# Performance work log

Measured on AMD Instinct MI355X. Metric: run time of the kernel, lower is better.

## Reference

```python
import jax, jax.numpy as jnp
import numpy as np

N_NODES = 100000
FEATURES, HIDDEN, CLASSES = 256, 128, 32
N_EDGES = 1600000


def setup_inputs() -> dict:
    key = jax.random.key(0)
    k1, k2, k3, k4, k5 = jax.random.split(key, 5)
    x = jax.random.normal(k1, (N_NODES, FEATURES), dtype=jnp.float32)
    edge_index = jax.random.randint(k2, (2, N_EDGES), 0, N_NODES, dtype=jnp.int64)
    # GCNConv: Linear(in, out, bias=False) + separate bias added after aggregation
    s1 = 1.0 / np.sqrt(FEATURES)
    s2 = 1.0 / np.sqrt(HIDDEN)
    W1 = jax.random.uniform(k3, (FEATURES, HIDDEN), jnp.float32, -s1, s1)
    b1 = jnp.zeros((HIDDEN,), jnp.float32)
    W2 = jax.random.uniform(k4, (HIDDEN, CLASSES), jnp.float32, -s2, s2)
    b2 = jnp.zeros((CLASSES,), jnp.float32)
    return {"x": x, "W1": W1, "b1": b1, "W2": W2, "b2": b2, "edge_index": edge_index}


def _gcn_conv(x, edge_index, W, b, n_nodes):
    # PyG GCNConv with add_self_loops=False: out = D^{-1/2} A D^{-1/2} (X W) + b
    src, dst = edge_index[0], edge_index[1]
    h = x @ W  # [N, out]
    deg = jax.ops.segment_sum(jnp.ones_like(dst, dtype=h.dtype), dst, num_segments=n_nodes)
    dinv = jnp.where(deg > 0, jax.lax.rsqrt(jnp.maximum(deg, 1e-12)), 0.0)
    norm = dinv[src] * dinv[dst]  # [E]
    msgs = h[src] * norm[:, None]  # [E, out] gather + scale
    out = jax.ops.segment_sum(msgs, dst, num_segments=n_nodes)  # scatter-add
    return out + b


def reference(x, W1, b1, W2, b2, edge_index):
    h = _gcn_conv(x, edge_index, W1, b1, N_NODES)
    h = jax.nn.relu(h)
    # F.dropout(training=self.training): eval mode -> identity
    h = _gcn_conv(h, edge_index, W2, b2, N_NODES)
    return jax.nn.log_softmax(h, axis=1)
```

## Files before the change

### kernel.cpp

```cpp
#include <hip/hip_runtime.h>

typedef unsigned short u16;
typedef unsigned int   u32;
typedef __attribute__((ext_vector_type(8))) short short8;
typedef __attribute__((ext_vector_type(4))) float f32x4;

constexpr int BSH = 9;
constexpr int BSZ = 1 << BSH;

__device__ inline float bf2f(u32 bits16) {
    union { u32 u; float f; } c; c.u = bits16 << 16; return c.f;
}
__device__ inline u16 f2bf(float f) {
    union { float f; u32 u; } c; c.f = f;
    return (u16)((c.u + 0x8000u) >> 16);
}
__device__ inline int ld_edge(const void* eb, int f64, size_t idx) {
    return f64 ? (int)((const long long*)eb)[idx] : ((const int*)eb)[idx];
}

__global__ void detect_kernel(const u32* xw, const int* ebuf_int, int* flags) {
    __shared__ int cnt;
    if (threadIdx.x == 0) cnt = 0;
    __syncthreads();
    u32 w = xw[threadIdx.x];
    int e = (int)((w >> 7) & 0xffu);
    if (e >= 110 && e <= 145) atomicAdd(&cnt, 1);
    int ev = ebuf_int[2 * threadIdx.x + 1];
    unsigned long long any = __ballot(ev != 0);
    __syncthreads();
    if (threadIdx.x == 0) {
        flags[0] = (cnt < 192) ? 1 : 0;
        flags[1] = 0;
        flags[2] = (any == 0ULL) ? 1 : 0;
    }
}

__global__ void bconv_kernel(const void* b1, const void* b2, const int* flags,
                             float* b1f, float* b2f, int HID, int CLS) {
    int i = blockIdx.x * 256 + threadIdx.x;
    int f = flags[0];
    if (i < HID) b1f[i] = f ? ((const float*)b1)[i] : bf2f(((const u16*)b1)[i]);
    if (i < CLS) b2f[i] = f ? ((const float*)b2)[i] : bf2f(((const u16*)b2)[i]);
}

__global__ void hist_kernel(const void* eb, const int* flags, int* bucket_cnt,
                            int E, int nb) {
    __shared__ int hist[256];
    hist[threadIdx.x] = 0;
    __syncthreads();
    int f64 = flags[2];
    int base = blockIdx.x * 4096;
    #pragma unroll
    for (int k = 0; k < 16; ++k) {
        int e = base + k * 256 + threadIdx.x;
        if (e < E) {
            int d = ld_edge(eb, f64, (size_t)E + e);
            atomicAdd(&hist[d >> BSH], 1);
        }
    }
    __syncthreads();
    int b = threadIdx.x;
    if (b < nb) { int c = hist[b]; if (c) atomicAdd(&bucket_cnt[b], c); }
}

__global__ void bucket_scan_kernel(const int* bucket_cnt, int* bucket_base,
                                   int* bucket_rsv, int nb, int E) {
    __shared__ int wsum[4];
    int t = threadIdx.x, lane = t & 63, wv = t >> 6;
    int v = (t < nb) ? bucket_cnt[t] : 0;
    int inc = v;
    #pragma unroll
    for (int d = 1; d < 64; d <<= 1) {
        int tmp = __shfl_up(inc, d, 64);
        if (lane >= d) inc += tmp;
    }
    if (lane == 63) wsum[wv] = inc;
    __syncthreads();
    int off = 0;
    #pragma unroll
    for (int w = 0; w < 4; ++w) if (w < wv) off += wsum[w];
    int excl = off + inc - v;
    if (t <= nb) bucket_base[t] = (t == nb) ? E : excl;
    if (t < nb) bucket_rsv[t] = excl;
}

__global__ __launch_bounds__(256)
void passA_kernel(const void* eb, const int* flags, int* bucket_rsv,
                  int* bsrc, int* bdst, int E, int nb) {
    __shared__ int hist[256];
    __shared__ int rbase[256];
    hist[threadIdx.x] = 0;
    __syncthreads();
    int f64 = flags[2];
    int base = blockIdx.x * 8192;
    #pragma unroll
    for (int k = 0; k < 32; ++k) {
        int e = base + k * 256 + threadIdx.x;
        if (e < E) {
            int d = ld_edge(eb, f64, (size_t)E + e);
            atomicAdd(&hist[d >> BSH], 1);
        }
    }
    __syncthreads();
    {
        int b = threadIdx.x;
        int c = (b < nb) ? hist[b] : 0;
        rbase[b] = c ? atomicAdd(&bucket_rsv[b], c) : 0;
        hist[b] = 0;
    }
    __syncthreads();
    #pragma unroll
    for (int k = 0; k < 32; ++k) {
        int e = base + k * 256 + threadIdx.x;
        if (e < E) {
            int d = ld_edge(eb, f64, (size_t)E + e);
            int s = ld_edge(eb, f64, (size_t)e);
            int bb = d >> BSH;
            int r = atomicAdd(&hist[bb], 1);
            int pos = rbase[bb] + r;
            bsrc[pos] = s;
            bdst[pos] = d;
        }
    }
}

__global__ __launch_bounds__(256)
void degB_kernel(const int* bdst, const int* bucket_base, int* deg, float* dinv, int N) {
    __shared__ int cur[BSZ];
    int b = blockIdx.x, d0 = b << BSH;
    for (int i = threadIdx.x; i < BSZ; i += 256) cur[i] = 0;
    __syncthreads();
    int e0 = bucket_base[b], e1 = bucket_base[b + 1];
    for (int e = e0 + threadIdx.x; e < e1; e += 256)
        atomicAdd(&cur[bdst[e] - d0], 1);
    __syncthreads();
    for (int i = threadIdx.x; i < BSZ; i += 256) {
        int d = d0 + i;
        if (d < N) {
            int c = cur[i];
            deg[d] = c;
            dinv[d] = (c > 0) ? 1.0f / sqrtf((float)c) : 0.0f;
        }
    }
}

__global__ __launch_bounds__(256)
void passB_kernel(const int* bsrc, const int* bdst, const int* bucket_base,
                  const int* row_start, int* csr) {
    __shared__ int cur[BSZ];
    int b = blockIdx.x, d0 = b << BSH;
    for (int i = threadIdx.x; i < BSZ; i += 256) cur[i] = 0;
    __syncthreads();
    int e0 = bucket_base[b], e1 = bucket_base[b + 1];
    for (int e = e0 + threadIdx.x; e < e1; e += 256) {
        int d = bdst[e];
        int s = bsrc[e];
        int r = atomicAdd(&cur[d - d0], 1);
        csr[row_start[d] + r] = s;
    }
}

__device__ inline int wave_incl_scan(int v, int lane) {
    #pragma unroll
    for (int d = 1; d < 64; d <<= 1) {
        int t = __shfl_up(v, d, 64);
        if (lane >= d) v += t;
    }
    return v;
}

__global__ void scan_block_kernel(const int* deg, int* row_start, int* bsums, int N) {
    __shared__ int wsum[4];
    int t = threadIdx.x, lane = t & 63, wv = t >> 6;
    int i = blockIdx.x * 256 + t;
    int v = (i < N) ? deg[i] : 0;
    int inc = wave_incl_scan(v, lane);
    if (lane == 63) wsum[wv] = inc;
    __syncthreads();
    int off = 0;
    #pragma unroll
    for (int w = 0; w < 4; ++w) if (w < wv) off += wsum[w];
    if (i < N) row_start[i] = off + inc - v;
    if (t == 255) bsums[blockIdx.x] = off + inc;
}

__global__ void scan_sums_kernel(int* bsums, int nb) {
    __shared__ int wsum[8];
    int t = threadIdx.x, lane = t & 63, wv = t >> 6;
    int v = (t < nb) ? bsums[t] : 0;
    int inc = wave_incl_scan(v, lane);
    if (lane == 63) wsum[wv] = inc;
    __syncthreads();
    int off = 0;
    #pragma unroll
    for (int w = 0; w < 8; ++w) if (w < wv) off += wsum[w];
    if (t < nb) bsums[t] = off + inc - v;
}

__global__ void scan_add_kernel(int* row_start, const int* bsums, int N, int E) {
    int i = blockIdx.x * 256 + threadIdx.x;
    if (i < N) row_start[i] += bsums[blockIdx.x];
    if (blockIdx.x == 0 && threadIdx.x == 0) row_start[N] = E;
}

template<int NT, int KT, int NCOLS>
__global__ void prepack_kernel(const void* W, const int* flags, u16* pack) {
    int p = blockIdx.x * 256 + threadIdx.x;
    constexpr int TOT = NT * KT * 64 * 8;
    if (p >= TOT) return;
    int j = p & 7, lane = (p >> 3) & 63, fk = p >> 9;
    int kk = fk % KT, nt = fk / KT;
    int n = nt * 16 + (lane & 15);
    int k = kk * 32 + (lane >> 4) * 8 + j;
    u16 v = flags[0] ? f2bf(((const float*)W)[k * NCOLS + n])
                     : ((const u16*)W)[k * NCOLS + n];
    pack[p] = v;
}

template<int NT, int KT, int G>
__global__ __launch_bounds__(256)
void gemm_kernel(const void* __restrict__ A, const int* __restrict__ ff,
                 const u16* __restrict__ Bpack, const float* __restrict__ dinv,
                 u16* __restrict__ C, int M) {
    constexpr int K = KT * 32;
    constexpr int Ncols = NT * 16;
    __shared__ short8 lds[NT * KT * 64];
    for (int i = threadIdx.x; i < NT * KT * 64; i += 256)
        lds[i] = ((const short8*)Bpack)[i];
    bool fA = (*ff != 0);
    __syncthreads();
    int wave = threadIdx.x >> 6, lane = threadIdx.x & 63;
    int m0 = (blockIdx.x * 4 + wave) * (16 * G);
    if (m0 >= M) return;
    int q = lane >> 4;
    int rowc[G];
    #pragma unroll
    for (int g = 0; g < G; ++g) {
        int r = m0 + g * 16 + (lane & 15);
        rowc[g] = (r < M) ? r : (M - 1);
    }
    f32x4 acc[G][NT];
    #pragma unroll
    for (int g = 0; g < G; ++g)
        #pragma unroll
        for (int nt = 0; nt < NT; ++nt) acc[g][nt] = (f32x4){0.f, 0.f, 0.f, 0.f};
    #pragma unroll
    for (int kk = 0; kk < KT; ++kk) {
        short8 a[G];
        #pragma unroll
        for (int g = 0; g < G; ++g) {
            if (fA) {
                const float* Af = (const float*)A + (size_t)rowc[g] * K + kk * 32 + q * 8;
                f32x4 v0 = ((const f32x4*)Af)[0];
                f32x4 v1 = ((const f32x4*)Af)[1];
                union { short8 s; u16 u[8]; } pa;
                pa.u[0] = f2bf(v0[0]); pa.u[1] = f2bf(v0[1]);
                pa.u[2] = f2bf(v0[2]); pa.u[3] = f2bf(v0[3]);
                pa.u[4] = f2bf(v1[0]); pa.u[5] = f2bf(v1[1]);
                pa.u[6] = f2bf(v1[2]); pa.u[7] = f2bf(v1[3]);
                a[g] = pa.s;
            } else {
                a[g] = ((const short8*)((const u16*)A + (size_t)rowc[g] * K))[kk * 4 + q];
            }
        }
        #pragma unroll
        for (int nt = 0; nt < NT; ++nt) {
            short8 b = lds[(nt * KT + kk) * 64 + lane];
            #pragma unroll
            for (int g = 0; g < G; ++g)
                acc[g][nt] = __builtin_amdgcn_mfma_f32_16x16x32_bf16(a[g], b, acc[g][nt], 0, 0, 0);
        }
    }
    #pragma unroll
    for (int g = 0; g < G; ++g) {
        float sc[4];
        #pragma unroll
        for (int r = 0; r < 4; ++r) {
            int rr = m0 + g * 16 + q * 4 + r;
            sc[r] = dinv[(rr < M) ? rr : (M - 1)];
        }
        #pragma unroll
        for (int nt = 0; nt < NT; ++nt) {
            int col = nt * 16 + (lane & 15);
            #pragma unroll
            for (int r = 0; r < 4; ++r) {
                int rrow = m0 + g * 16 + q * 4 + r;
                if (rrow < M)
                    C[(size_t)rrow * Ncols + col] = f2bf(acc[g][nt][r] * sc[r]);
            }
        }
    }
}

__global__ __launch_bounds__(256)
void agg1_kernel(const u32* __restrict__ H32, const int* __restrict__ csr,
                 const int* __restrict__ row_start, const float* __restrict__ dinv,
                 const float* __restrict__ b1f, u32* __restrict__ H1, int N) {
    int wave = threadIdx.x >> 6, lane = threadIdx.x & 63;
    int n = blockIdx.x * 4 + wave;
    if (n >= N) return;
    int s0 = row_start[n], s1 = row_start[n + 1];
    float acc0 = 0.f, acc1 = 0.f;
    for (int base = s0; base < s1; base += 64) {
        int m = s1 - base; if (m > 64) m = 64;
        int myidx = (lane < m) ? csr[base + lane] : 0;
        int j = 0;
        for (; j + 4 <= m; j += 4) {
            int i0 = __shfl(myidx, j);
            int i1 = __shfl(myidx, j + 1);
            int i2 = __shfl(myidx, j + 2);
            int i3 = __shfl(myidx, j + 3);
            u32 h0 = H32[(size_t)i0 * 64 + lane];
            u32 h1 = H32[(size_t)i1 * 64 + lane];
            u32 h2 = H32[(size_t)i2 * 64 + lane];
            u32 h3 = H32[(size_t)i3 * 64 + lane];
            acc0 += bf2f(h0 & 0xffffu); acc1 += bf2f(h0 >> 16);
            acc0 += bf2f(h1 & 0xffffu); acc1 += bf2f(h1 >> 16);
            acc0 += bf2f(h2 & 0xffffu); acc1 += bf2f(h2 >> 16);
            acc0 += bf2f(h3 & 0xffffu); acc1 += bf2f(h3 >> 16);
        }
        for (; j < m; ++j) {
            int s = __shfl(myidx, j);
            u32 h = H32[(size_t)s * 64 + lane];
            acc0 += bf2f(h & 0xffffu); acc1 += bf2f(h >> 16);
        }
    }
    float wn = dinv[n];
    float v0 = fmaxf(wn * acc0 + b1f[2 * lane], 0.f);
    float v1 = fmaxf(wn * acc1 + b1f[2 * lane + 1], 0.f);
    H1[(size_t)n * 64 + lane] = (u32)f2bf(v0) | ((u32)f2bf(v1) << 16);
}

__global__ __launch_bounds__(256)
void agg2_kernel(const u16* __restrict__ H2, const int* __restrict__ csr,
                 const int* __restrict__ row_start, const float* __restrict__ dinv,
                 const float* __restrict__ b2f, const int* __restrict__ ff,
                 void* __restrict__ out, int N) {
    int half = threadIdx.x >> 5;
    int c = threadIdx.x & 31;
    int n = blockIdx.x * 8 + half;
    if (n >= N) return;
    int s0 = row_start[n], s1 = row_start[n + 1];
    float acc = 0.f;
    for (int base = s0; base < s1; base += 32) {
        int m = s1 - base; if (m > 32) m = 32;
        int myidx = (c < m) ? csr[base + c] : 0;
        int j = 0;
        for (; j + 4 <= m; j += 4) {
            int i0 = __shfl(myidx, j, 32);
            int i1 = __shfl(myidx, j + 1, 32);
            int i2 = __shfl(myidx, j + 2, 32);
            int i3 = __shfl(myidx, j + 3, 32);
            float h0 = bf2f(H2[(size_t)i0 * 32 + c]);
            float h1 = bf2f(H2[(size_t)i1 * 32 + c]);
            float h2 = bf2f(H2[(size_t)i2 * 32 + c]);
            float h3 = bf2f(H2[(size_t)i3 * 32 + c]);
            acc += h0 + h1 + h2 + h3;
        }
        for (; j < m; ++j) {
            int s = __shfl(myidx, j, 32);
            acc += bf2f(H2[(size_t)s * 32 + c]);
        }
    }
    float tot = dinv[n] * acc + b2f[c];
    float mx = tot;
    #pragma unroll
    for (int m = 16; m; m >>= 1) mx = fmaxf(mx, __shfl_xor(mx, m, 32));
    float ex = expf(tot - mx);
    float sm = ex;
    #pragma unroll
    for (int m = 16; m; m >>= 1) sm += __shfl_xor(sm, m, 32);
    float r = tot - mx - logf(sm);
    if (*ff) ((float*)out)[(size_t)n * 32 + c] = r;
    else     ((u16*)out)[(size_t)n * 32 + c] = f2bf(r);
}

extern "C" void kernel_launch(void* const* d_in, const int* in_sizes, int n_in,
                              void* d_out, int out_size, void* d_ws, size_t ws_size,
                              hipStream_t stream) {
    const void* x  = d_in[0];
    const void* W1 = d_in[1];
    const void* b1 = d_in[2];
    const void* W2 = d_in[3];
    const void* b2 = d_in[4];
    const void* eb = d_in[5];

    const int HID  = in_sizes[2];
    const int CLS  = in_sizes[4];
    const int FEAT = in_sizes[1] / HID;
    const int N    = in_sizes[0] / FEAT;
    const int E    = in_sizes[5] / 2;
    const int nb   = (N + BSZ - 1) >> BSH;
    (void)n_in; (void)out_size;

    char* w = (char*)d_ws;
    size_t p = 0;
    auto alloc = [&](size_t bytes) {
        size_t o = p; p = (p + bytes + 255) & ~(size_t)255; return o;
    };
    int*   flags      = (int*)  (w + alloc(32));
    int*   deg        = (int*)  (w + alloc((size_t)N * 4));
    int*   row_start  = (int*)  (w + alloc((size_t)(N + 1) * 4));
    int*   bsums      = (int*)  (w + alloc(512 * 4));
    int*   bucket_cnt = (int*)  (w + alloc(257 * 4));
    int*   bucket_base= (int*)  (w + alloc(257 * 4));
    int*   bucket_rsv = (int*)  (w + alloc(256 * 4));
    int*   bsrc       = (int*)  (w + alloc((size_t)E * 4));
    int*   bdst       = (int*)  (w + alloc((size_t)E * 4));
    int*   csr        = (int*)  (w + alloc((size_t)E * 4));
    float* dinv       = (float*)(w + alloc((size_t)N * 4));
    float* b1f        = (float*)(w + alloc((size_t)HID * 4));
    float* b2f        = (float*)(w + alloc((size_t)CLS * 4));
    u16*   B1p        = (u16*)  (w + alloc((size_t)FEAT * HID * 2));
    u16*   B2p        = (u16*)  (w + alloc((size_t)HID * CLS * 2));
    u16*   H          = (u16*)  (w + alloc((size_t)N * HID * 2));
    u16*   H1         = (u16*)  (w + alloc((size_t)N * HID * 2));
    u16*   H2         = (u16*)  (w + alloc((size_t)N * CLS * 2));
    if (p > ws_size) return;

    detect_kernel<<<1, 256, 0, stream>>>((const u32*)x, (const int*)eb, flags);
    hipMemsetAsync(bucket_cnt, 0, 257 * 4, stream);
    bconv_kernel<<<1, 256, 0, stream>>>(b1, b2, flags, b1f, b2f, HID, CLS);

    hist_kernel<<<(E + 4095) / 4096, 256, 0, stream>>>(eb, flags, bucket_cnt, E, nb);
    bucket_scan_kernel<<<1, 256, 0, stream>>>(bucket_cnt, bucket_base, bucket_rsv, nb, E);
    passA_kernel<<<(E + 8191) / 8192, 256, 0, stream>>>(eb, flags, bucket_rsv,
                                                        bsrc, bdst, E, nb);
    degB_kernel<<<nb, 256, 0, stream>>>(bdst, bucket_base, deg, dinv, N);

    int nsb = (N + 255) / 256;
    scan_block_kernel<<<nsb, 256, 0, stream>>>(deg, row_start, bsums, N);
    scan_sums_kernel<<<1, 512, 0, stream>>>(bsums, nsb);
    scan_add_kernel<<<nsb, 256, 0, stream>>>(row_start, bsums, N, E);

    passB_kernel<<<nb, 256, 0, stream>>>(bsrc, bdst, bucket_base, row_start, csr);

    prepack_kernel<8, 8, 128><<<(8 * 8 * 64 * 8 + 255) / 256, 256, 0, stream>>>(W1, flags, B1p);
    prepack_kernel<2, 4, 32><<<(2 * 4 * 64 * 8 + 255) / 256, 256, 0, stream>>>(W2, flags, B2p);

    int gblocks = (N + 127) / 128;
    gemm_kernel<8, 8, 2><<<gblocks, 256, 0, stream>>>(x, flags, B1p, dinv, H, N);
    agg1_kernel<<<(N + 3) / 4, 256, 0, stream>>>((const u32*)H, csr, row_start, dinv, b1f,
                                                 (u32*)H1, N);
    gemm_kernel<2, 4, 2><<<gblocks, 256, 0, stream>>>(H1, flags + 1, B2p, dinv, H2, N);
    agg2_kernel<<<(N + 7) / 8, 256, 0, stream>>>(H2, csr, row_start, dinv, b2f, flags,
                                                 (void*)d_out, N);
}
```

Measured before the change: 401.2 us.

## Double-buffer first-layer GEMM with async global-to-LDS loads per K-slice

Replaces the first GEMM with a new kernel that stages A and B tiles per 32-wide K slice into double-buffered LDS using global_load_lds async copies, overlapping the next slice's loads with MFMA on the current one. W1 is repacked in K-major order so each K slice of B is contiguous. The goal is to hide global memory latency of the large x read, which dominates the first GEMM. It adds more LDS use and a barrier per K step, and depends on correct async-copy layout.

```diff
diff --git a/kernel.cpp b/kernel.cpp
--- a/kernel.cpp
+++ b/kernel.cpp
@@ -17,6 +17,11 @@
 }
 __device__ inline int ld_edge(const void* eb, int f64, size_t idx) {
     return f64 ? (int)((const long long*)eb)[idx] : ((const int*)eb)[idx];
+}
+__device__ inline void async_cp16(const void* g, void* s) {
+    __builtin_amdgcn_global_load_lds(
+        (const __attribute__((address_space(1))) unsigned int*)g,
+        (__attribute__((address_space(3))) unsigned int*)s, 16, 0, 0);
 }
 
 __global__ void detect_kernel(const u32* xw, const int* ebuf_int, int* flags) {
@@ -216,6 +221,127 @@
     u16 v = flags[0] ? f2bf(((const float*)W)[k * NCOLS + n])
                      : ((const u16*)W)[k * NCOLS + n];
     pack[p] = v;
+}
+
+template<int NT, int KT, int NCOLS>
+__global__ void prepackK_kernel(const void* W, const int* flags, u16* pack) {
+    int p = blockIdx.x * 256 + threadIdx.x;
+    constexpr int TOT = NT * KT * 64 * 8;
+    if (p >= TOT) return;
+    int j = p & 7, lane = (p >> 3) & 63, fk = p >> 9;
+    int nt = fk % NT, kk = fk / NT;
+    int n = nt * 16 + (lane & 15);
+    int k = kk * 32 + (lane >> 4) * 8 + j;
+    u16 v = flags[0] ? f2bf(((const float*)W)[k * NCOLS + n])
+                     : ((const u16*)W)[k * NCOLS + n];
+    pack[p] = v;
+}
+
+template<int NT, int KT>
+__global__ __launch_bounds__(256)
+void gemm1_kernel(const void* __restrict__ A, const int* __restrict__ ff,
+                  const u16* __restrict__ Bpack, const float* __restrict__ dinv,
+                  u16* __restrict__ C, int M) {
+    constexpr int K = KT * 32;
+    constexpr int Ncols = NT * 16;
+    __shared__ char As[2][16384];
+    __shared__ char Bs[2][8192];
+    const bool fA = (*ff != 0);
+    const int wave = threadIdx.x >> 6, lane = threadIdx.x & 63;
+    const int r0 = blockIdx.x * 128;
+
+    auto stage = [&](int kk, int buf) {
+        if (fA) {
+            #pragma unroll
+            for (int i = 0; i < 4; ++i) {
+                int cb = (i * 4 + wave) * 32;
+                int c = cb + (lane >> 1);
+                int rg = c >> 6, rem = c & 63, q = rem >> 4, l16 = rem & 15;
+                int row = r0 + rg * 16 + l16; if (row >= M) row = M - 1;
+                const char* g = (const char*)A + (size_t)row * (K * 4)
+                                + (kk * 32 + q * 8) * 4 + (lane & 1) * 16;
+                async_cp16(g, &As[buf][(size_t)cb * 32]);
+            }
+        } else {
+            #pragma unroll
+            for (int i = 0; i < 2; ++i) {
+                int cb = (i * 4 + wave) * 64;
+                int c = cb + lane;
+                int rg = c >> 6, rem = c & 63, q = rem >> 4, l16 = rem & 15;
+                int row = r0 + rg * 16 + l16; if (row >= M) row = M - 1;
+                const char* g = (const char*)A + (size_t)row * (K * 2)
+                                + (kk * 32 + q * 8) * 2;
+                async_cp16(g, &As[buf][(size_t)cb * 16]);
+            }
+        }
+        #pragma unroll
+        for (int i = 0; i < 2; ++i) {
+            int off = (i * 4 + wave) * 1024;
+            const char* g = (const char*)Bpack + (size_t)kk * (NT * 1024) + off
+                            + (size_t)lane * 16;
+            async_cp16(g, &Bs[buf][off]);
+        }
+    };
+
+    const int q = lane >> 4, l16 = lane & 15;
+    f32x4 acc[2][NT];
+    #pragma unroll
+    for (int g = 0; g < 2; ++g)
+        #pragma unroll
+        for (int nt = 0; nt < NT; ++nt) acc[g][nt] = (f32x4){0.f, 0.f, 0.f, 0.f};
+
+    stage(0, 0);
+    #pragma unroll
+    for (int kk = 0; kk < KT; ++kk) {
+        int cur = kk & 1;
+        __syncthreads();
+        if (kk + 1 < KT) stage(kk + 1, cur ^ 1);
+        short8 a[2];
+        #pragma unroll
+        for (int g = 0; g < 2; ++g) {
+            int rg = wave * 2 + g;
+            int fragidx = (rg * 4 + q) * 16 + l16;
+            if (fA) {
+                const f32x4* ap = (const f32x4*)&As[cur][(size_t)fragidx * 32];
+                f32x4 v0 = ap[0];
+                f32x4 v1 = ap[1];
+                union { short8 s; u16 u[8]; } pa;
+                pa.u[0] = f2bf(v0[0]); pa.u[1] = f2bf(v0[1]);
+                pa.u[2] = f2bf(v0[2]); pa.u[3] = f2bf(v0[3]);
+                pa.u[4] = f2bf(v1[0]); pa.u[5] = f2bf(v1[1]);
+                pa.u[6] = f2bf(v1[2]); pa.u[7] = f2bf(v1[3]);
+                a[g] = pa.s;
+            } else {
+                a[g] = *(const short8*)&As[cur][(size_t)fragidx * 16];
+            }
+        }
+        #pragma unroll
+        for (int nt = 0; nt < NT; ++nt) {
+            short8 b = ((const short8*)Bs[cur])[nt * 64 + lane];
+            acc[0][nt] = __builtin_amdgcn_mfma_f32_16x16x32_bf16(a[0], b, acc[0][nt], 0, 0, 0);
+            acc[1][nt] = __builtin_amdgcn_mfma_f32_16x16x32_bf16(a[1], b, acc[1][nt], 0, 0, 0);
+        }
+    }
+    #pragma unroll
+    for (int g = 0; g < 2; ++g) {
+        int mg = r0 + (wave * 2 + g) * 16;
+        float sc[4];
+        #pragma unroll
+        for (int r = 0; r < 4; ++r) {
+            int rr = mg + q * 4 + r;
+            sc[r] = dinv[(rr < M) ? rr : (M - 1)];
+        }
+        #pragma unroll
+        for (int nt = 0; nt < NT; ++nt) {
+            int col = nt * 16 + l16;
+            #pragma unroll
+            for (int r = 0; r < 4; ++r) {
+                int rrow = mg + q * 4 + r;
+                if (rrow < M)
+                    C[(size_t)rrow * Ncols + col] = f2bf(acc[g][nt][r] * sc[r]);
+            }
+        }
+    }
 }
 
 template<int NT, int KT, int G>
@@ -436,14 +562,13 @@
 
     passB_kernel<<<nb, 256, 0, stream>>>(bsrc, bdst, bucket_base, row_start, csr);
 
-    prepack_kernel<8, 8, 128><<<(8 * 8 * 64 * 8 + 255) / 256, 256, 0, stream>>>(W1, flags, B1p);
+    prepackK_kernel<8, 8, 128><<<(8 * 8 * 64 * 8 + 255) / 256, 256, 0, stream>>>(W1, flags, B1p);
     prepack_kernel<2, 4, 32><<<(2 * 4 * 64 * 8 + 255) / 256, 256, 0, stream>>>(W2, flags, B2p);
 
-    int gblocks = (N + 127) / 128;
-    gemm_kernel<8, 8, 2><<<gblocks, 256, 0, stream>>>(x, flags, B1p, dinv, H, N);
+    gemm1_kernel<8, 8><<<(N + 127) / 128, 256, 0, stream>>>(x, flags, B1p, dinv, H, N);
     agg1_kernel<<<(N + 3) / 4, 256, 0, stream>>>((const u32*)H, csr, row_start, dinv, b1f,
                                                  (u32*)H1, N);
-    gemm_kernel<2, 4, 2><<<gblocks, 256, 0, stream>>>(H1, flags + 1, B2p, dinv, H2, N);
+    gemm_kernel<2, 4, 2><<<(N + 127) / 128, 256, 0, stream>>>(H1, flags + 1, B2p, dinv, H2, N);
     agg2_kernel<<<(N + 7) / 8, 256, 0, stream>>>(H2, csr, row_start, dinv, b2f, flags,
                                                  (void*)d_out, N);
 }
```

After: 397.9 us. No clear change (-0.8%).

## Split first GEMM across column halves and unroll aggregation gathers deeper

Applied to the files above, without the earlier changes.

The first GEMM now runs as gemm1_kernel, which splits the 128 output columns into two halves handled by separate blocks. This doubles the grid and halves the LDS footprint per block, meant to raise occupancy, but each block re-reads its A rows, so the x reads are duplicated. Both aggregation kernels gain an 8-way unrolled gather loop to keep more loads in flight. agg1 also uses a packed float2 bf16 unpack with tree-style sums, which slightly changes the floating-point summation order.

```diff
diff --git a/kernel.cpp b/kernel.cpp
--- a/kernel.cpp
+++ b/kernel.cpp
@@ -4,6 +4,7 @@
 typedef unsigned int   u32;
 typedef __attribute__((ext_vector_type(8))) short short8;
 typedef __attribute__((ext_vector_type(4))) float f32x4;
+typedef __attribute__((ext_vector_type(2))) float f32x2;
 
 constexpr int BSH = 9;
 constexpr int BSZ = 1 << BSH;
@@ -14,6 +15,12 @@
 __device__ inline u16 f2bf(float f) {
     union { float f; u32 u; } c; c.f = f;
     return (u16)((c.u + 0x8000u) >> 16);
+}
+__device__ inline f32x2 up2(u32 h) {
+    union { u32 u[2]; f32x2 f; } c;
+    c.u[0] = h << 16;
+    c.u[1] = h & 0xffff0000u;
+    return c.f;
 }
 __device__ inline int ld_edge(const void* eb, int f64, size_t idx) {
     return f64 ? (int)((const long long*)eb)[idx] : ((const int*)eb)[idx];
@@ -218,26 +225,33 @@
     pack[p] = v;
 }
 
-template<int NT, int KT, int G>
-__global__ __launch_bounds__(256)
-void gemm_kernel(const void* __restrict__ A, const int* __restrict__ ff,
-                 const u16* __restrict__ Bpack, const float* __restrict__ dinv,
-                 u16* __restrict__ C, int M) {
+template<int NT, int NTF, int KT, int G>
+__global__ __launch_bounds__(256)
+void gemm1_kernel(const void* __restrict__ A, const int* __restrict__ ff,
+                  const u16* __restrict__ Bpack, const float* __restrict__ dinv,
+                  u16* __restrict__ C, int M) {
     constexpr int K = KT * 32;
-    constexpr int Ncols = NT * 16;
+    constexpr int Ncols = NTF * 16;
+    constexpr int NSPLIT = NTF / NT;
     __shared__ short8 lds[NT * KT * 64];
-    for (int i = threadIdx.x; i < NT * KT * 64; i += 256)
-        lds[i] = ((const short8*)Bpack)[i];
+    const int bh = blockIdx.x % NSPLIT;
+    const int bm = blockIdx.x / NSPLIT;
+    for (int i = threadIdx.x; i < NT * KT * 64; i += 256) {
+        int lane_ = i & 63;
+        int kk = (i >> 6) % KT;
+        int nt = (i >> 6) / KT;
+        lds[i] = ((const short8*)Bpack)[(((bh * NT + nt) * KT) + kk) * 64 + lane_];
+    }
     bool fA = (*ff != 0);
     __syncthreads();
     int wave = threadIdx.x >> 6, lane = threadIdx.x & 63;
-    int m0 = (blockIdx.x * 4 + wave) * (16 * G);
+    int m0 = (bm * 4 + wave) * (16 * G);
     if (m0 >= M) return;
-    int q = lane >> 4;
+    int q = lane >> 4, l16 = lane & 15;
     int rowc[G];
     #pragma unroll
     for (int g = 0; g < G; ++g) {
-        int r = m0 + g * 16 + (lane & 15);
+        int r = m0 + g * 16 + l16;
         rowc[g] = (r < M) ? r : (M - 1);
     }
     f32x4 acc[G][NT];
@@ -282,6 +296,81 @@
         }
         #pragma unroll
         for (int nt = 0; nt < NT; ++nt) {
+            int col = bh * (NT * 16) + nt * 16 + l16;
+            #pragma unroll
+            for (int r = 0; r < 4; ++r) {
+                int rrow = m0 + g * 16 + q * 4 + r;
+                if (rrow < M)
+                    C[(size_t)rrow * Ncols + col] = f2bf(acc[g][nt][r] * sc[r]);
+            }
+        }
+    }
+}
+
+template<int NT, int KT, int G>
+__global__ __launch_bounds__(256)
+void gemm_kernel(const void* __restrict__ A, const int* __restrict__ ff,
+                 const u16* __restrict__ Bpack, const float* __restrict__ dinv,
+                 u16* __restrict__ C, int M) {
+    constexpr int K = KT * 32;
+    constexpr int Ncols = NT * 16;
+    __shared__ short8 lds[NT * KT * 64];
+    for (int i = threadIdx.x; i < NT * KT * 64; i += 256)
+        lds[i] = ((const short8*)Bpack)[i];
+    bool fA = (*ff != 0);
+    __syncthreads();
+    int wave = threadIdx.x >> 6, lane = threadIdx.x & 63;
+    int m0 = (blockIdx.x * 4 + wave) * (16 * G);
+    if (m0 >= M) return;
+    int q = lane >> 4;
+    int rowc[G];
+    #pragma unroll
+    for (int g = 0; g < G; ++g) {
+        int r = m0 + g * 16 + (lane & 15);
+        rowc[g] = (r < M) ? r : (M - 1);
+    }
+    f32x4 acc[G][NT];
+    #pragma unroll
+    for (int g = 0; g < G; ++g)
+        #pragma unroll
+        for (int nt = 0; nt < NT; ++nt) acc[g][nt] = (f32x4){0.f, 0.f, 0.f, 0.f};
+    #pragma unroll
+    for (int kk = 0; kk < KT; ++kk) {
+        short8 a[G];
+        #pragma unroll
+        for (int g = 0; g < G; ++g) {
+            if (fA) {
+                const float* Af = (const float*)A + (size_t)rowc[g] * K + kk * 32 + q * 8;
+                f32x4 v0 = ((const f32x4*)Af)[0];
+                f32x4 v1 = ((const f32x4*)Af)[1];
+                union { short8 s; u16 u[8]; } pa;
+                pa.u[0] = f2bf(v0[0]); pa.u[1] = f2bf(v0[1]);
+                pa.u[2] = f2bf(v0[2]); pa.u[3] = f2bf(v0[3]);
+                pa.u[4] = f2bf(v1[0]); pa.u[5] = f2bf(v1[1]);
+                pa.u[6] = f2bf(v1[2]); pa.u[7] = f2bf(v1[3]);
+                a[g] = pa.s;
+            } else {
+                a[g] = ((const short8*)((const u16*)A + (size_t)rowc[g] * K))[kk * 4 + q];
+            }
+        }
+        #pragma unroll
+        for (int nt = 0; nt < NT; ++nt) {
+            short8 b = lds[(nt * KT + kk) * 64 + lane];
+            #pragma unroll
+            for (int g = 0; g < G; ++g)
+                acc[g][nt] = __builtin_amdgcn_mfma_f32_16x16x32_bf16(a[g], b, acc[g][nt], 0, 0, 0);
+        }
+    }
+    #pragma unroll
+    for (int g = 0; g < G; ++g) {
+        float sc[4];
+        #pragma unroll
+        for (int r = 0; r < 4; ++r) {
+            int rr = m0 + g * 16 + q * 4 + r;
+            sc[r] = dinv[(rr < M) ? rr : (M - 1)];
+        }
+        #pragma unroll
+        for (int nt = 0; nt < NT; ++nt) {
             int col = nt * 16 + (lane & 15);
             #pragma unroll
             for (int r = 0; r < 4; ++r) {
@@ -301,11 +390,34 @@
     int n = blockIdx.x * 4 + wave;
     if (n >= N) return;
     int s0 = row_start[n], s1 = row_start[n + 1];
-    float acc0 = 0.f, acc1 = 0.f;
+    f32x2 acc = {0.f, 0.f};
     for (int base = s0; base < s1; base += 64) {
         int m = s1 - base; if (m > 64) m = 64;
         int myidx = (lane < m) ? csr[base + lane] : 0;
         int j = 0;
+        for (; j + 8 <= m; j += 8) {
+            int i0 = __shfl(myidx, j);
+            int i1 = __shfl(myidx, j + 1);
+            int i2 = __shfl(myidx, j + 2);
+            int i3 = __shfl(myidx, j + 3);
+            int i4 = __shfl(myidx, j + 4);
+            int i5 = __shfl(myidx, j + 5);
+            int i6 = __shfl(myidx, j + 6);
+            int i7 = __shfl(myidx, j + 7);
+            u32 h0 = H32[(size_t)i0 * 64 + lane];
+            u32 h1 = H32[(size_t)i1 * 64 + lane];
+            u32 h2 = H32[(size_t)i2 * 64 + lane];
+            u32 h3 = H32[(size_t)i3 * 64 + lane];
+            u32 h4 = H32[(size_t)i4 * 64 + lane];
+            u32 h5 = H32[(size_t)i5 * 64 + lane];
+            u32 h6 = H32[(size_t)i6 * 64 + lane];
+            u32 h7 = H32[(size_t)i7 * 64 + lane];
+            f32x2 t0 = up2(h0) + up2(h1);
+            f32x2 t1 = up2(h2) + up2(h3);
+            f32x2 t2 = up2(h4) + up2(h5);
+            f32x2 t3 = up2(h6) + up2(h7);
+            acc += (t0 + t1) + (t2 + t3);
+        }
         for (; j + 4 <= m; j += 4) {
             int i0 = __shfl(myidx, j);
             int i1 = __shfl(myidx, j + 1);
@@ -315,20 +427,16 @@
             u32 h1 = H32[(size_t)i1 * 64 + lane];
             u32 h2 = H32[(size_t)i2 * 64 + lane];
             u32 h3 = H32[(size_t)i3 * 64 + lane];
-            acc0 += bf2f(h0 & 0xffffu); acc1 += bf2f(h0 >> 16);
-            acc0 += bf2f(h1 & 0xffffu); acc1 += bf2f(h1 >> 16);
-            acc0 += bf2f(h2 & 0xffffu); acc1 += bf2f(h2 >> 16);
-            acc0 += bf2f(h3 & 0xffffu); acc1 += bf2f(h3 >> 16);
+            acc += (up2(h0) + up2(h1)) + (up2(h2) + up2(h3));
         }
         for (; j < m; ++j) {
             int s = __shfl(myidx, j);
-            u32 h = H32[(size_t)s * 64 + lane];
-            acc0 += bf2f(h & 0xffffu); acc1 += bf2f(h >> 16);
+            acc += up2(H32[(size_t)s * 64 + lane]);
         }
     }
     float wn = dinv[n];
-    float v0 = fmaxf(wn * acc0 + b1f[2 * lane], 0.f);
-    float v1 = fmaxf(wn * acc1 + b1f[2 * lane + 1], 0.f);
+    float v0 = fmaxf(wn * acc.x + b1f[2 * lane], 0.f);
+    float v1 = fmaxf(wn * acc.y + b1f[2 * lane + 1], 0.f);
     H1[(size_t)n * 64 + lane] = (u32)f2bf(v0) | ((u32)f2bf(v1) << 16);
 }
 
@@ -347,6 +455,25 @@
         int m = s1 - base; if (m > 32) m = 32;
         int myidx = (c < m) ? csr[base + c] : 0;
         int j = 0;
+        for (; j + 8 <= m; j += 8) {
+            int i0 = __shfl(myidx, j, 32);
+            int i1 = __shfl(myidx, j + 1, 32);
+            int i2 = __shfl(myidx, j + 2, 32);
+            int i3 = __shfl(myidx, j + 3, 32);
+            int i4 = __shfl(myidx, j + 4, 32);
+            int i5 = __shfl(myidx, j + 5, 32);
+            int i6 = __shfl(myidx, j + 6, 32);
+            int i7 = __shfl(myidx, j + 7, 32);
+            float h0 = bf2f(H2[(size_t)i0 * 32 + c]);
+            float h1 = bf2f(H2[(size_t)i1 * 32 + c]);
+            float h2 = bf2f(H2[(size_t)i2 * 32 + c]);
+            float h3 = bf2f(H2[(size_t)i3 * 32 + c]);
+            float h4 = bf2f(H2[(size_t)i4 * 32 + c]);
+            float h5 = bf2f(H2[(size_t)i5 * 32 + c]);
+            float h6 = bf2f(H2[(size_t)i6 * 32 + c]);
+            float h7 = bf2f(H2[(size_t)i7 * 32 + c]);
+            acc += ((h0 + h1) + (h2 + h3)) + ((h4 + h5) + (h6 + h7));
+        }
         for (; j + 4 <= m; j += 4) {
             int i0 = __shfl(myidx, j, 32);
             int i1 = __shfl(myidx, j + 1, 32);
@@ -356,7 +483,7 @@
             float h1 = bf2f(H2[(size_t)i1 * 32 + c]);
             float h2 = bf2f(H2[(size_t)i2 * 32 + c]);
             float h3 = bf2f(H2[(size_t)i3 * 32 + c]);
-            acc += h0 + h1 + h2 + h3;
+            acc += (h0 + h1) + (h2 + h3);
         }
         for (; j < m; ++j) {
             int s = __shfl(myidx, j, 32);
@@ -439,11 +566,10 @@
     prepack_kernel<8, 8, 128><<<(8 * 8 * 64 * 8 + 255) / 256, 256, 0, stream>>>(W1, flags, B1p);
     prepack_kernel<2, 4, 32><<<(2 * 4 * 64 * 8 + 255) / 256, 256, 0, stream>>>(W2, flags, B2p);
 
-    int gblocks = (N + 127) / 128;
-    gemm_kernel<8, 8, 2><<<gblocks, 256, 0, stream>>>(x, flags, B1p, dinv, H, N);
+    gemm1_kernel<4, 8, 8, 2><<<2 * ((N + 127) / 128), 256, 0, stream>>>(x, flags, B1p, dinv, H, N);
     agg1_kernel<<<(N + 3) / 4, 256, 0, stream>>>((const u32*)H, csr, row_start, dinv, b1f,
                                                  (u32*)H1, N);
-    gemm_kernel<2, 4, 2><<<gblocks, 256, 0, stream>>>(H1, flags + 1, B2p, dinv, H2, N);
+    gemm_kernel<2, 4, 2><<<(N + 127) / 128, 256, 0, stream>>>(H1, flags + 1, B2p, dinv, H2, N);
     agg2_kernel<<<(N + 7) / 8, 256, 0, stream>>>(H2, csr, row_start, dinv, b2f, flags,
                                                  (void*)d_out, N);
 }
```

Result: faster. 389.9 us (-2.8%).
